# Kernel optimization log

Hardware: AMD Instinct MI355X
Metric: run time of the kernel (lower is better)

The kernel has to match this reference:

```python
import jax, jax.numpy as jnp
import numpy as np

DIM = 64
N_NEIGHBOR = 32
N_ENTITY = 1_000_000
N_RELATION = 64
N_USER = 500_000
BATCH = 16384


def _xavier_uniform(key, shape):
    fan_in, fan_out = shape[0], shape[1]
    bound = float(np.sqrt(6.0 / (fan_in + fan_out)))
    return jax.random.uniform(key, shape, jnp.float32, -bound, bound)


def setup_inputs() -> dict:
    key = jax.random.key(0)
    ks = jax.random.split(key, 10)
    users = jax.random.randint(ks[0], (BATCH,), 0, N_USER)
    items = jax.random.randint(ks[1], (BATCH,), 0, N_ENTITY)
    label = jnp.round(jax.random.uniform(ks[2], (BATCH,), jnp.float32))
    neighbor_rel = jax.random.randint(ks[3], (BATCH, N_NEIGHBOR), 0, N_RELATION)
    neighbor_tail = jax.random.randint(ks[4], (BATCH, N_NEIGHBOR), 0, N_ENTITY)
    user_emb = _xavier_uniform(ks[5], (N_USER, DIM))
    entity_emb = _xavier_uniform(ks[6], (N_ENTITY, DIM))
    relation_emb = _xavier_uniform(ks[7], (N_RELATION, DIM))
    in_dim = 2 * N_NEIGHBOR * DIM
    wb = float(np.sqrt(1.0 / in_dim))  # torch Linear default init bound
    gen_W = jax.random.uniform(ks[8], (DIM, in_dim), jnp.float32, -wb, wb)
    gen_b = jax.random.uniform(ks[9], (DIM,), jnp.float32, -wb, wb)
    return {"users": users, "items": items, "label": label,
            "neighbor_rel": neighbor_rel, "neighbor_tail": neighbor_tail,
            "user_emb": user_emb, "entity_emb": entity_emb,
            "relation_emb": relation_emb, "gen_W": gen_W, "gen_b": gen_b}


def _bce(p, y):
    # torch BCELoss: clamps log terms at -100, mean reduction
    logp = jnp.clip(jnp.log(p), -100.0)
    log1mp = jnp.clip(jnp.log1p(-p), -100.0)
    return -jnp.mean(y * logp + (1.0 - y) * log1mp)


def reference(users, items, label, neighbor_rel, neighbor_tail,
              user_emb, entity_emb, relation_emb, gen_W, gen_b):
    u = user_emb[users]                       # [B, D]
    i = entity_emb[items]                     # [B, D]
    predict = jax.nn.sigmoid(jnp.sum(u * i, axis=1))

    rel = relation_emb[neighbor_rel]          # [B, K, D]
    tail = entity_emb[neighbor_tail]          # [B, K, D]
    t_r = jnp.concatenate([rel, tail], axis=-1).reshape(u.shape[0], -1)  # [B, 2*K*D]
    false_item = jax.nn.sigmoid(t_r @ gen_W.T + gen_b)                   # [B, D]
    false_predict = jax.nn.sigmoid(jnp.sum(u * false_item, axis=1))

    return _bce(predict, label) + _bce(false_predict, label)
```

## Files before the change

### kernel.cpp

```cpp
#include <hip/hip_runtime.h>
#include <hip/hip_bf16.h>

#define BATCH 16384
#define DIM   64
#define NNB   32
#define INDIM 4096
#define BR    16
#define WPB   4
#define NPW   (NNB / WPB)
#define NBLK  (BATCH / BR)

typedef __attribute__((ext_vector_type(8))) short          s16x8;
typedef __attribute__((ext_vector_type(4))) float          f32x4;
typedef __attribute__((ext_vector_type(4))) unsigned short u16x4;

__device__ __forceinline__ float bf2f(unsigned short u) {
    union { unsigned int i; float f; } v;
    v.i = ((unsigned int)u) << 16;
    return v.f;
}

template<bool FP32>
__device__ __forceinline__ float ldT(const void* p, size_t i) {
    if constexpr (FP32) return ((const float*)p)[i];
    else                return bf2f(((const unsigned short*)p)[i]);
}

template<bool FP32>
__device__ __forceinline__ f32x4 ld4(const void* p, size_t i) {
    if constexpr (FP32) {
        return *(const f32x4*)((const float*)p + i);
    } else {
        const u16x4 v = *(const u16x4*)((const unsigned short*)p + i);
        f32x4 r;
        #pragma unroll
        for (int j = 0; j < 4; ++j) r[j] = bf2f(v[j]);
        return r;
    }
}

__device__ __forceinline__ void split8(const f32x4 x, const f32x4 y, s16x8& h, s16x8& l) {
    #pragma unroll
    for (int j = 0; j < 8; ++j) {
        const float v = (j < 4) ? x[j] : y[j - 4];
        union { float f; unsigned u; } a, b, c;
        a.f = v;
        const unsigned short hh = (unsigned short)(a.u >> 16);
        b.u = ((unsigned)hh) << 16;
        c.f = v - b.f;
        h[j] = (short)hh;
        l[j] = (short)(c.u >> 16);
    }
}

__global__ void kgnn_probe(const unsigned int* __restrict__ lab, int* __restrict__ flag) {
    if (threadIdx.x == 0) {
        int ok = 1;
        for (int i = 0; i < 32; ++i) {
            unsigned int w = lab[i];
            if (!(w == 0u || w == 0x3F800000u)) ok = 0;
        }
        *flag = ok;
    }
}

template<bool FP32>
__global__ __launch_bounds__(256, 4) void kgnn_gemm(
    const int* __restrict__ users, const int* __restrict__ items,
    const void* __restrict__ label_, const int* __restrict__ nrel,
    const int* __restrict__ ntail,  const void* __restrict__ uemb_,
    const void* __restrict__ eemb_, const void* __restrict__ remb_,
    const void* __restrict__ W_,    const void* __restrict__ b_,
    double* __restrict__ acc, double* __restrict__ bsum,
    const int* __restrict__ flag, const int force)
{
    if (force < 0 && *flag != (FP32 ? 1 : 0)) return;

    __shared__ float fl[WPB][BR][68];
    __shared__ float st[BR];

    const int t    = threadIdx.x;
    const int base = blockIdx.x * BR;
    const int lane = t & 63;
    const int w    = t >> 6;
    const int r16  = lane & 15;
    const int kg   = lane >> 4;
    const int n0   = w * NPW;

    int pr0, pr1, pt0, pt1;
    {
        const size_t rb = (size_t)(base + r16) * NNB + n0;
        pr0 = nrel [rb + kg];
        pr1 = nrel [rb + 4 + kg];
        pt0 = ntail[rb + kg];
        pt1 = ntail[rb + 4 + kg];
    }

    f32x4 ac[4] = { {0,0,0,0}, {0,0,0,0}, {0,0,0,0}, {0,0,0,0} };

    if constexpr (!FP32) {
        const unsigned short* E = (const unsigned short*)eemb_;
        const unsigned short* R = (const unsigned short*)remb_;
        const unsigned short* W = (const unsigned short*)W_;
        #pragma unroll 2
        for (int q = 0; q < NPW; ++q) {
            const int n    = n0 + q;
            const int ridx = __shfl((q & 4) ? pr1 : pr0, r16 + 16 * (q & 3), 64);
            const int tidx = __shfl((q & 4) ? pt1 : pt0, r16 + 16 * (q & 3), 64);
            const unsigned short* rr = R + (size_t)ridx * DIM + kg * 8;
            const unsigned short* tr = E + (size_t)tidx * DIM + kg * 8;
            const s16x8 a0 = *(const s16x8*)(rr);
            const s16x8 a1 = *(const s16x8*)(rr + 32);
            const s16x8 a2 = *(const s16x8*)(tr);
            const s16x8 a3 = *(const s16x8*)(tr + 32);
            const unsigned short* wq = W + (size_t)r16 * INDIM + n * 128 + kg * 8;
            #pragma unroll
            for (int dt = 0; dt < 4; ++dt) {
                const unsigned short* wd = wq + (size_t)dt * 16 * INDIM;
                const s16x8 b0 = *(const s16x8*)(wd);
                const s16x8 b1 = *(const s16x8*)(wd + 32);
                const s16x8 b2 = *(const s16x8*)(wd + 64);
                const s16x8 b3 = *(const s16x8*)(wd + 96);
                ac[dt] = __builtin_amdgcn_mfma_f32_16x16x32_bf16(a0, b0, ac[dt], 0, 0, 0);
                ac[dt] = __builtin_amdgcn_mfma_f32_16x16x32_bf16(a1, b1, ac[dt], 0, 0, 0);
                ac[dt] = __builtin_amdgcn_mfma_f32_16x16x32_bf16(a2, b2, ac[dt], 0, 0, 0);
                ac[dt] = __builtin_amdgcn_mfma_f32_16x16x32_bf16(a3, b3, ac[dt], 0, 0, 0);
            }
        }
    } else {
        const float* E = (const float*)eemb_;
        const float* R = (const float*)remb_;
        const float* W = (const float*)W_;
        #pragma unroll 2
        for (int q = 0; q < NPW; ++q) {
            const int n    = n0 + q;
            const int ridx = __shfl((q & 4) ? pr1 : pr0, r16 + 16 * (q & 3), 64);
            const int tidx = __shfl((q & 4) ? pt1 : pt0, r16 + 16 * (q & 3), 64);
            const float* rr = R + (size_t)ridx * DIM + kg * 8;
            const float* tr = E + (size_t)tidx * DIM + kg * 8;
            s16x8 ah[4], al[4];
            #pragma unroll
            for (int s = 0; s < 4; ++s) {
                const float* ap = (s < 2) ? rr + s * 32 : tr + (s - 2) * 32;
                split8(*(const f32x4*)(ap), *(const f32x4*)(ap + 4), ah[s], al[s]);
            }
            const float* wq = W + (size_t)r16 * INDIM + n * 128 + kg * 8;
            #pragma unroll
            for (int dt = 0; dt < 4; ++dt) {
                const float* wd = wq + (size_t)dt * 16 * INDIM;
                #pragma unroll
                for (int s = 0; s < 4; ++s) {
                    s16x8 bh, bl;
                    split8(*(const f32x4*)(wd + s * 32), *(const f32x4*)(wd + s * 32 + 4),
                           bh, bl);
                    ac[dt] = __builtin_amdgcn_mfma_f32_16x16x32_bf16(ah[s], bh, ac[dt], 0, 0, 0);
                    ac[dt] = __builtin_amdgcn_mfma_f32_16x16x32_bf16(ah[s], bl, ac[dt], 0, 0, 0);
                    ac[dt] = __builtin_amdgcn_mfma_f32_16x16x32_bf16(al[s], bh, ac[dt], 0, 0, 0);
                }
            }
        }
    }

    #pragma unroll
    for (int dt = 0; dt < 4; ++dt)
        #pragma unroll
        for (int qq = 0; qq < 4; ++qq)
            fl[w][kg * 4 + qq][dt * 16 + r16] = ac[dt][qq];
    __syncthreads();

    {
        const int row  = t >> 4;
        const int c    = t & 15;
        const int grow = base + row;
        const int uid  = users[grow], iid = items[grow];
        const f32x4 uv = ld4<FP32>(uemb_, (size_t)uid * DIM + c * 4);
        const f32x4 iv = ld4<FP32>(eemb_, (size_t)iid * DIM + c * 4);
        const f32x4 bv = ld4<FP32>(b_, (size_t)c * 4);
        float p1 = 0.f, p2 = 0.f;
        #pragma unroll
        for (int j = 0; j < 4; ++j) {
            const int d = c * 4 + j;
            const float lg = fl[0][row][d] + fl[1][row][d]
                           + fl[2][row][d] + fl[3][row][d] + bv[j];
            const float fi = 1.f / (1.f + expf(-lg));
            p2 += uv[j] * fi;
            p1 += uv[j] * iv[j];
        }
        #pragma unroll
        for (int m = 1; m < 16; m <<= 1) {
            p1 += __shfl_xor(p1, m, 16);
            p2 += __shfl_xor(p2, m, 16);
        }
        if (c == 0) {
            const float y  = ldT<FP32>(label_, grow);
            const float pa = 1.f / (1.f + expf(-p1));
            const float pb = 1.f / (1.f + expf(-p2));
            st[row] =
                  y * fmaxf(logf(pa), -100.f) + (1.f - y) * fmaxf(log1pf(-pa), -100.f)
                + y * fmaxf(logf(pb), -100.f) + (1.f - y) * fmaxf(log1pf(-pb), -100.f);
        }
    }
    __syncthreads();

    if (t < 64) {
        float s = (t < BR) ? st[t] : 0.f;
        #pragma unroll
        for (int m = 1; m < 64; m <<= 1) s += __shfl_xor(s, m, 64);
        if (t == 0) {
            if (bsum) bsum[blockIdx.x] = (double)s;
            else      atomicAdd(acc, (double)s);
        }
    }
}

__global__ void kgnn_fin(const double* __restrict__ acc, const double* __restrict__ bsum,
                         const int* __restrict__ flag, void* __restrict__ out,
                         const int mode) {
    __shared__ double sd[4];
    const int t = threadIdx.x;
    double s = 0.0;
    if (bsum) {
        for (int i = t; i < NBLK; i += 256) s += bsum[i];
    } else if (t == 0) {
        s = *acc;
    }
    #pragma unroll
    for (int m = 1; m < 64; m <<= 1) s += __shfl_xor(s, m, 64);
    if ((t & 63) == 0) sd[t >> 6] = s;
    __syncthreads();
    if (t == 0) {
        const double tot = sd[0] + sd[1] + sd[2] + sd[3];
        const int md = (mode < 0) ? *flag : mode;
        const float loss = (float)(-tot / (double)BATCH);
        if (md) ((float*)out)[0] = loss;
        else    ((__hip_bfloat16*)out)[0] = __float2bfloat16(loss);
    }
}

extern "C" void kernel_launch(void* const* d_in, const int* in_sizes, int n_in,
                              void* d_out, int out_size, void* d_ws, size_t ws_size,
                              hipStream_t stream) {
    const int* users = (const int*)d_in[0];
    const int* items = (const int*)d_in[1];
    const void* label = d_in[2];
    const int* nrel  = (const int*)d_in[3];
    const int* ntail = (const int*)d_in[4];
    const void* uemb = d_in[5];
    const void* eemb = d_in[6];
    const void* remb = d_in[7];
    const void* genW = d_in[8];
    const void* genb = d_in[9];

    double* acc  = (double*)d_ws;
    int*    flag = (int*)((char*)d_ws + 8);
    double* bsum = (ws_size >= (size_t)(16 + NBLK * 8))
                       ? (double*)((char*)d_ws + 16) : nullptr;
    hipMemsetAsync(d_ws, 0, 16, stream);

    const bool f32sz  = (out_size == 4) && (in_sizes[5] == 128000000);
    const bool bf16sz = (out_size == 2) && (in_sizes[5] == 64000000);

    if (f32sz) {
        kgnn_gemm<true><<<NBLK, 256, 0, stream>>>(
            users, items, label, nrel, ntail, uemb, eemb, remb, genW, genb,
            acc, bsum, flag, 1);
        kgnn_fin<<<1, 256, 0, stream>>>(acc, bsum, flag, d_out, 1);
    } else if (bf16sz) {
        kgnn_gemm<false><<<NBLK, 256, 0, stream>>>(
            users, items, label, nrel, ntail, uemb, eemb, remb, genW, genb,
            acc, bsum, flag, 0);
        kgnn_fin<<<1, 256, 0, stream>>>(acc, bsum, flag, d_out, 0);
    } else {
        kgnn_probe<<<1, 64, 0, stream>>>((const unsigned int*)label, flag);
        kgnn_gemm<false><<<NBLK, 256, 0, stream>>>(
            users, items, label, nrel, ntail, uemb, eemb, remb, genW, genb,
            acc, bsum, flag, -1);
        kgnn_gemm<true><<<NBLK, 256, 0, stream>>>(
            users, items, label, nrel, ntail, uemb, eemb, remb, genW, genb,
            acc, bsum, flag, -1);
        kgnn_fin<<<1, 256, 0, stream>>>(acc, bsum, flag, d_out, -1);
    }
}
```

Baseline: 509.9 us.

## Split GEMM over K slices with LDS-staged W and separate epilogue kernel

New measurement: 430.7 us. 1.18x faster.

```diff
diff --git a/kernel.cpp b/kernel.cpp
--- a/kernel.cpp
+++ b/kernel.cpp
@@ -5,13 +5,12 @@
 #define DIM   64
 #define NNB   32
 #define INDIM 4096
-#define BR    16
-#define WPB   4
-#define NPW   (NNB / WPB)
-#define NBLK  (BATCH / BR)
+#define RPB   128
+#define EPB   1024
 
 typedef __attribute__((ext_vector_type(8))) short          s16x8;
 typedef __attribute__((ext_vector_type(4))) float          f32x4;
+typedef __attribute__((ext_vector_type(4))) unsigned int   u32x4;
 typedef __attribute__((ext_vector_type(4))) unsigned short u16x4;
 
 __device__ __forceinline__ float bf2f(unsigned short u) {
@@ -65,7 +64,182 @@
 }
 
 template<bool FP32>
-__global__ __launch_bounds__(256, 4) void kgnn_gemm(
+__global__ __launch_bounds__(512, 4) void kgnn_part(
+    const int* __restrict__ nrel, const int* __restrict__ ntail,
+    const void* __restrict__ eemb_, const void* __restrict__ remb_,
+    const void* __restrict__ W_,
+    float* __restrict__ part, const int* __restrict__ flag, const int force)
+{
+    if (force < 0 && *flag != (FP32 ? 1 : 0)) return;
+
+    constexpr int NSL = FP32 ? 2 : 4;
+    constexpr int NS  = FP32 ? 16 : 8;
+    __shared__ __align__(16) unsigned char ldsW[65536];
+
+    const int t     = threadIdx.x;
+    const int bid   = blockIdx.x;
+    const int slice = bid & (NS - 1);
+    const int rtile = bid / NS;
+    const int base  = rtile * RPB;
+    const int lane  = t & 63;
+    const int w     = t >> 6;
+    const int r16   = lane & 15;
+    const int kg    = lane >> 4;
+    const int sw    = (r16 & 7) << 4;
+
+    if constexpr (!FP32) {
+        const unsigned char* Wb = (const unsigned char*)W_;
+        #pragma unroll
+        for (int i = 0; i < 8; ++i) {
+            const int e = i * 512 + t;
+            const int dim = e >> 6, ko = (e & 63) * 16;
+            const u32x4 v = *(const u32x4*)(Wb + (size_t)dim * 8192 + slice * 1024 + ko);
+            *(u32x4*)&ldsW[dim * 1024 + (ko ^ ((dim & 7) << 4))] = v;
+        }
+    } else {
+        const float* Wf = (const float*)W_;
+        #pragma unroll
+        for (int i = 0; i < 4; ++i) {
+            const int e = i * 512 + t;
+            const int dim = e >> 5, g = e & 31;
+            const float* src = Wf + (size_t)dim * INDIM + slice * 256 + g * 8;
+            s16x8 h, l;
+            split8(*(const f32x4*)src, *(const f32x4*)(src + 4), h, l);
+            const int swd = (dim & 7) << 4;
+            *(s16x8*)&ldsW[dim * 1024 + ((g * 16) ^ swd)]       = h;
+            *(s16x8*)&ldsW[dim * 1024 + ((512 + g * 16) ^ swd)] = l;
+        }
+    }
+
+    const size_t rb = (size_t)(base + w * 16 + r16) * NNB + slice * NSL;
+    const int pr = nrel [rb + (kg % NSL)];
+    const int pt = ntail[rb + (kg % NSL)];
+
+    __syncthreads();
+
+    f32x4 ac[4] = { {0,0,0,0}, {0,0,0,0}, {0,0,0,0}, {0,0,0,0} };
+
+    if constexpr (!FP32) {
+        const unsigned short* E = (const unsigned short*)eemb_;
+        const unsigned short* R = (const unsigned short*)remb_;
+        #pragma unroll 2
+        for (int q = 0; q < NSL; ++q) {
+            const int ridx = __shfl(pr, r16 + 16 * q, 64);
+            const int tidx = __shfl(pt, r16 + 16 * q, 64);
+            const unsigned short* rr = R + (size_t)ridx * DIM + kg * 8;
+            const unsigned short* tr = E + (size_t)tidx * DIM + kg * 8;
+            s16x8 a[4];
+            a[0] = *(const s16x8*)(rr);
+            a[1] = *(const s16x8*)(rr + 32);
+            a[2] = *(const s16x8*)(tr);
+            a[3] = *(const s16x8*)(tr + 32);
+            #pragma unroll
+            for (int dt = 0; dt < 4; ++dt) {
+                const int rowb = (dt * 16 + r16) * 1024;
+                #pragma unroll
+                for (int ks = 0; ks < 4; ++ks) {
+                    const s16x8 b = *(const s16x8*)
+                        &ldsW[rowb + ((q * 256 + ks * 64 + kg * 16) ^ sw)];
+                    ac[dt] = __builtin_amdgcn_mfma_f32_16x16x32_bf16(a[ks], b, ac[dt], 0, 0, 0);
+                }
+            }
+        }
+    } else {
+        const float* E = (const float*)eemb_;
+        const float* R = (const float*)remb_;
+        #pragma unroll
+        for (int q = 0; q < NSL; ++q) {
+            const int ridx = __shfl(pr, r16 + 16 * q, 64);
+            const int tidx = __shfl(pt, r16 + 16 * q, 64);
+            const float* rr = R + (size_t)ridx * DIM + kg * 8;
+            const float* tr = E + (size_t)tidx * DIM + kg * 8;
+            s16x8 ah[4], al[4];
+            #pragma unroll
+            for (int s = 0; s < 4; ++s) {
+                const float* ap = (s < 2) ? rr + s * 32 : tr + (s - 2) * 32;
+                split8(*(const f32x4*)(ap), *(const f32x4*)(ap + 4), ah[s], al[s]);
+            }
+            #pragma unroll
+            for (int dt = 0; dt < 4; ++dt) {
+                const int rowb = (dt * 16 + r16) * 1024;
+                #pragma unroll
+                for (int ks = 0; ks < 4; ++ks) {
+                    const int ko = q * 256 + ks * 64 + kg * 16;
+                    const s16x8 bh = *(const s16x8*)&ldsW[rowb + (ko ^ sw)];
+                    const s16x8 bl = *(const s16x8*)&ldsW[rowb + ((512 + ko) ^ sw)];
+                    ac[dt] = __builtin_amdgcn_mfma_f32_16x16x32_bf16(ah[ks], bh, ac[dt], 0, 0, 0);
+                    ac[dt] = __builtin_amdgcn_mfma_f32_16x16x32_bf16(ah[ks], bl, ac[dt], 0, 0, 0);
+                    ac[dt] = __builtin_amdgcn_mfma_f32_16x16x32_bf16(al[ks], bh, ac[dt], 0, 0, 0);
+                }
+            }
+        }
+    }
+
+    #pragma unroll
+    for (int dt = 0; dt < 4; ++dt)
+        #pragma unroll
+        for (int qq = 0; qq < 4; ++qq) {
+            const int row = base + w * 16 + kg * 4 + qq;
+            part[((size_t)row * NS + slice) * 64 + dt * 16 + r16] = ac[dt][qq];
+        }
+}
+
+template<bool FP32>
+__global__ void kgnn_epi(
+    const int* __restrict__ users, const int* __restrict__ items,
+    const void* __restrict__ label_, const void* __restrict__ uemb_,
+    const void* __restrict__ eemb_, const void* __restrict__ b_,
+    const float* __restrict__ part, double* __restrict__ bsum,
+    const int* __restrict__ flag, const int force)
+{
+    if (force < 0 && *flag != (FP32 ? 1 : 0)) return;
+    constexpr int NS = FP32 ? 16 : 8;
+    __shared__ float st[16];
+
+    const int t   = threadIdx.x;
+    const int row = blockIdx.x * 16 + (t >> 4);
+    const int c   = t & 15;
+
+    f32x4 fs = {0.f, 0.f, 0.f, 0.f};
+    #pragma unroll
+    for (int sl = 0; sl < NS; ++sl)
+        fs += *(const f32x4*)(part + ((size_t)row * NS + sl) * 64 + c * 4);
+
+    const int uid = users[row], iid = items[row];
+    const f32x4 uv = ld4<FP32>(uemb_, (size_t)uid * DIM + c * 4);
+    const f32x4 iv = ld4<FP32>(eemb_, (size_t)iid * DIM + c * 4);
+    const f32x4 bv = ld4<FP32>(b_, (size_t)c * 4);
+    float p1 = 0.f, p2 = 0.f;
+    #pragma unroll
+    for (int j = 0; j < 4; ++j) {
+        const float fi = 1.f / (1.f + expf(-(fs[j] + bv[j])));
+        p2 += uv[j] * fi;
+        p1 += uv[j] * iv[j];
+    }
+    #pragma unroll
+    for (int m = 1; m < 16; m <<= 1) {
+        p1 += __shfl_xor(p1, m, 16);
+        p2 += __shfl_xor(p2, m, 16);
+    }
+    if (c == 0) {
+        const float y  = ldT<FP32>(label_, row);
+        const float pa = 1.f / (1.f + expf(-p1));
+        const float pb = 1.f / (1.f + expf(-p2));
+        st[t >> 4] =
+              y * fmaxf(logf(pa), -100.f) + (1.f - y) * fmaxf(log1pf(-pa), -100.f)
+            + y * fmaxf(logf(pb), -100.f) + (1.f - y) * fmaxf(log1pf(-pb), -100.f);
+    }
+    __syncthreads();
+    if (t < 64) {
+        float s = (t < 16) ? st[t] : 0.f;
+        #pragma unroll
+        for (int m = 1; m < 64; m <<= 1) s += __shfl_xor(s, m, 64);
+        if (t == 0) bsum[blockIdx.x] = (double)s;
+    }
+}
+
+template<bool FP32>
+__global__ __launch_bounds__(256, 4) void kgnn_fb(
     const int* __restrict__ users, const int* __restrict__ items,
     const void* __restrict__ label_, const int* __restrict__ nrel,
     const int* __restrict__ ntail,  const void* __restrict__ uemb_,
@@ -75,56 +249,39 @@
     const int* __restrict__ flag, const int force)
 {
     if (force < 0 && *flag != (FP32 ? 1 : 0)) return;
-
-    __shared__ float fl[WPB][BR][68];
-    __shared__ float st[BR];
-
-    const int t    = threadIdx.x;
-    const int base = blockIdx.x * BR;
-    const int lane = t & 63;
-    const int w    = t >> 6;
-    const int r16  = lane & 15;
-    const int kg   = lane >> 4;
-    const int n0   = w * NPW;
-
+    __shared__ float fl[4][16][68];
+    __shared__ float st[16];
+    const int t = threadIdx.x, base = blockIdx.x * 16;
+    const int lane = t & 63, w = t >> 6, r16 = lane & 15, kg = lane >> 4;
+    const int n0 = w * 8;
     int pr0, pr1, pt0, pt1;
     {
         const size_t rb = (size_t)(base + r16) * NNB + n0;
-        pr0 = nrel [rb + kg];
-        pr1 = nrel [rb + 4 + kg];
-        pt0 = ntail[rb + kg];
-        pt1 = ntail[rb + 4 + kg];
-    }
-
+        pr0 = nrel[rb + kg];  pr1 = nrel[rb + 4 + kg];
+        pt0 = ntail[rb + kg]; pt1 = ntail[rb + 4 + kg];
+    }
     f32x4 ac[4] = { {0,0,0,0}, {0,0,0,0}, {0,0,0,0}, {0,0,0,0} };
-
     if constexpr (!FP32) {
         const unsigned short* E = (const unsigned short*)eemb_;
         const unsigned short* R = (const unsigned short*)remb_;
         const unsigned short* W = (const unsigned short*)W_;
         #pragma unroll 2
-        for (int q = 0; q < NPW; ++q) {
-            const int n    = n0 + q;
+        for (int q = 0; q < 8; ++q) {
+            const int n = n0 + q;
             const int ridx = __shfl((q & 4) ? pr1 : pr0, r16 + 16 * (q & 3), 64);
             const int tidx = __shfl((q & 4) ? pt1 : pt0, r16 + 16 * (q & 3), 64);
             const unsigned short* rr = R + (size_t)ridx * DIM + kg * 8;
             const unsigned short* tr = E + (size_t)tidx * DIM + kg * 8;
-            const s16x8 a0 = *(const s16x8*)(rr);
-            const s16x8 a1 = *(const s16x8*)(rr + 32);
-            const s16x8 a2 = *(const s16x8*)(tr);
-            const s16x8 a3 = *(const s16x8*)(tr + 32);
+            const s16x8 a0 = *(const s16x8*)(rr),      a1 = *(const s16x8*)(rr + 32);
+            const s16x8 a2 = *(const s16x8*)(tr),      a3 = *(const s16x8*)(tr + 32);
             const unsigned short* wq = W + (size_t)r16 * INDIM + n * 128 + kg * 8;
             #pragma unroll
             for (int dt = 0; dt < 4; ++dt) {
                 const unsigned short* wd = wq + (size_t)dt * 16 * INDIM;
-                const s16x8 b0 = *(const s16x8*)(wd);
-                const s16x8 b1 = *(const s16x8*)(wd + 32);
-                const s16x8 b2 = *(const s16x8*)(wd + 64);
-                const s16x8 b3 = *(const s16x8*)(wd + 96);
-                ac[dt] = __builtin_amdgcn_mfma_f32_16x16x32_bf16(a0, b0, ac[dt], 0, 0, 0);
-                ac[dt] = __builtin_amdgcn_mfma_f32_16x16x32_bf16(a1, b1, ac[dt], 0, 0, 0);
-                ac[dt] = __builtin_amdgcn_mfma_f32_16x16x32_bf16(a2, b2, ac[dt], 0, 0, 0);
-                ac[dt] = __builtin_amdgcn_mfma_f32_16x16x32_bf16(a3, b3, ac[dt], 0, 0, 0);
+                ac[dt] = __builtin_amdgcn_mfma_f32_16x16x32_bf16(a0, *(const s16x8*)(wd),      ac[dt], 0, 0, 0);
+                ac[dt] = __builtin_amdgcn_mfma_f32_16x16x32_bf16(a1, *(const s16x8*)(wd + 32), ac[dt], 0, 0, 0);
+                ac[dt] = __builtin_amdgcn_mfma_f32_16x16x32_bf16(a2, *(const s16x8*)(wd + 64), ac[dt], 0, 0, 0);
+                ac[dt] = __builtin_amdgcn_mfma_f32_16x16x32_bf16(a3, *(const s16x8*)(wd + 96), ac[dt], 0, 0, 0);
             }
         }
     } else {
@@ -132,8 +289,8 @@
         const float* R = (const float*)remb_;
         const float* W = (const float*)W_;
         #pragma unroll 2
-        for (int q = 0; q < NPW; ++q) {
-            const int n    = n0 + q;
+        for (int q = 0; q < 8; ++q) {
+            const int n = n0 + q;
             const int ridx = __shfl((q & 4) ? pr1 : pr0, r16 + 16 * (q & 3), 64);
             const int tidx = __shfl((q & 4) ? pt1 : pt0, r16 + 16 * (q & 3), 64);
             const float* rr = R + (size_t)ridx * DIM + kg * 8;
@@ -151,8 +308,7 @@
                 #pragma unroll
                 for (int s = 0; s < 4; ++s) {
                     s16x8 bh, bl;
-                    split8(*(const f32x4*)(wd + s * 32), *(const f32x4*)(wd + s * 32 + 4),
-                           bh, bl);
+                    split8(*(const f32x4*)(wd + s * 32), *(const f32x4*)(wd + s * 32 + 4), bh, bl);
                     ac[dt] = __builtin_amdgcn_mfma_f32_16x16x32_bf16(ah[s], bh, ac[dt], 0, 0, 0);
                     ac[dt] = __builtin_amdgcn_mfma_f32_16x16x32_bf16(ah[s], bl, ac[dt], 0, 0, 0);
                     ac[dt] = __builtin_amdgcn_mfma_f32_16x16x32_bf16(al[s], bh, ac[dt], 0, 0, 0);
@@ -160,19 +316,15 @@
             }
         }
     }
-
     #pragma unroll
     for (int dt = 0; dt < 4; ++dt)
         #pragma unroll
         for (int qq = 0; qq < 4; ++qq)
             fl[w][kg * 4 + qq][dt * 16 + r16] = ac[dt][qq];
     __syncthreads();
-
     {
-        const int row  = t >> 4;
-        const int c    = t & 15;
-        const int grow = base + row;
-        const int uid  = users[grow], iid = items[grow];
+        const int row = t >> 4, c = t & 15, grow = base + row;
+        const int uid = users[grow], iid = items[grow];
         const f32x4 uv = ld4<FP32>(uemb_, (size_t)uid * DIM + c * 4);
         const f32x4 iv = ld4<FP32>(eemb_, (size_t)iid * DIM + c * 4);
         const f32x4 bv = ld4<FP32>(b_, (size_t)c * 4);
@@ -180,10 +332,8 @@
         #pragma unroll
         for (int j = 0; j < 4; ++j) {
             const int d = c * 4 + j;
-            const float lg = fl[0][row][d] + fl[1][row][d]
-                           + fl[2][row][d] + fl[3][row][d] + bv[j];
-            const float fi = 1.f / (1.f + expf(-lg));
-            p2 += uv[j] * fi;
+            const float lg = fl[0][row][d] + fl[1][row][d] + fl[2][row][d] + fl[3][row][d] + bv[j];
+            p2 += uv[j] * (1.f / (1.f + expf(-lg)));
             p1 += uv[j] * iv[j];
         }
         #pragma unroll
@@ -201,9 +351,8 @@
         }
     }
     __syncthreads();
-
     if (t < 64) {
-        float s = (t < BR) ? st[t] : 0.f;
+        float s = (t < 16) ? st[t] : 0.f;
         #pragma unroll
         for (int m = 1; m < 64; m <<= 1) s += __shfl_xor(s, m, 64);
         if (t == 0) {
@@ -220,7 +369,7 @@
     const int t = threadIdx.x;
     double s = 0.0;
     if (bsum) {
-        for (int i = t; i < NBLK; i += 256) s += bsum[i];
+        for (int i = t; i < EPB; i += 256) s += bsum[i];
     } else if (t == 0) {
         s = *acc;
     }
@@ -253,31 +402,57 @@
 
     double* acc  = (double*)d_ws;
     int*    flag = (int*)((char*)d_ws + 8);
-    double* bsum = (ws_size >= (size_t)(16 + NBLK * 8))
-                       ? (double*)((char*)d_ws + 16) : nullptr;
+    double* bsum = (ws_size >= (size_t)(1024 + EPB * 8)) ? (double*)((char*)d_ws + 1024)
+                                                         : nullptr;
+    float*  part = (float*)((char*)d_ws + 16384);
+    const size_t needB = 16384 + (size_t)BATCH * 8  * 64 * 4;
+    const size_t needF = 16384 + (size_t)BATCH * 16 * 64 * 4;
     hipMemsetAsync(d_ws, 0, 16, stream);
 
     const bool f32sz  = (out_size == 4) && (in_sizes[5] == 128000000);
     const bool bf16sz = (out_size == 2) && (in_sizes[5] == 64000000);
 
-    if (f32sz) {
-        kgnn_gemm<true><<<NBLK, 256, 0, stream>>>(
+    if (f32sz && bsum && ws_size >= needF) {
+        kgnn_part<true><<<(BATCH / RPB) * 16, 512, 0, stream>>>(
+            nrel, ntail, eemb, remb, genW, part, flag, 1);
+        kgnn_epi<true><<<EPB, 256, 0, stream>>>(
+            users, items, label, uemb, eemb, genb, part, bsum, flag, 1);
+        kgnn_fin<<<1, 256, 0, stream>>>(acc, bsum, flag, d_out, 1);
+    } else if (bf16sz && bsum && ws_size >= needB) {
+        kgnn_part<false><<<(BATCH / RPB) * 8, 512, 0, stream>>>(
+            nrel, ntail, eemb, remb, genW, part, flag, 0);
+        kgnn_epi<false><<<EPB, 256, 0, stream>>>(
+            users, items, label, uemb, eemb, genb, part, bsum, flag, 0);
+        kgnn_fin<<<1, 256, 0, stream>>>(acc, bsum, flag, d_out, 0);
+    } else if (f32sz) {
+        kgnn_fb<true><<<EPB, 256, 0, stream>>>(
             users, items, label, nrel, ntail, uemb, eemb, remb, genW, genb,
             acc, bsum, flag, 1);
         kgnn_fin<<<1, 256, 0, stream>>>(acc, bsum, flag, d_out, 1);
     } else if (bf16sz) {
-        kgnn_gemm<false><<<NBLK, 256, 0, stream>>>(
+        kgnn_fb<false><<<EPB, 256, 0, stream>>>(
             users, items, label, nrel, ntail, uemb, eemb, remb, genW, genb,
             acc, bsum, flag, 0);
         kgnn_fin<<<1, 256, 0, stream>>>(acc, bsum, flag, d_out, 0);
     } else {
         kgnn_probe<<<1, 64, 0, stream>>>((const unsigned int*)label, flag);
-        kgnn_gemm<false><<<NBLK, 256, 0, stream>>>(
-            users, items, label, nrel, ntail, uemb, eemb, remb, genW, genb,
-            acc, bsum, flag, -1);
-        kgnn_gemm<true><<<NBLK, 256, 0, stream>>>(
-            users, items, label, nrel, ntail, uemb, eemb, remb, genW, genb,
-            acc, bsum, flag, -1);
+        if (bsum && ws_size >= needF) {
+            kgnn_part<false><<<(BATCH / RPB) * 8, 512, 0, stream>>>(
+                nrel, ntail, eemb, remb, genW, part, flag, -1);
+            kgnn_part<true><<<(BATCH / RPB) * 16, 512, 0, stream>>>(
+                nrel, ntail, eemb, remb, genW, part, flag, -1);
+            kgnn_epi<false><<<EPB, 256, 0, stream>>>(
+                users, items, label, uemb, eemb, genb, part, bsum, flag, -1);
+            kgnn_epi<true><<<EPB, 256, 0, stream>>>(
+                users, items, label, uemb, eemb, genb, part, bsum, flag, -1);
+        } else {
+            kgnn_fb<false><<<EPB, 256, 0, stream>>>(
+                users, items, label, nrel, ntail, uemb, eemb, remb, genW, genb,
+                acc, bsum, flag, -1);
+            kgnn_fb<true><<<EPB, 256, 0, stream>>>(
+                users, items, label, nrel, ntail, uemb, eemb, remb, genW, genb,
+                acc, bsum, flag, -1);
+        }
         kgnn_fin<<<1, 256, 0, stream>>>(acc, bsum, flag, d_out, -1);
     }
 }
```
